# Kernel tuning notes

Measured on AMD Instinct MI355X. Metric: run time of the kernel, lower is better.

Reference implementation:

```python
import jax, jax.numpy as jnp
import numpy as np

D_MODEL = 768
D_STATE = 16
D_CONV = 4
EXPAND = 2
D_INNER = EXPAND * D_MODEL  # 1536
DT_RANK = 48  # ceil(768/16)
D_FF = 3072
EPS = 1e-5


def layer_norm(x, g, b):
    mu = jnp.mean(x, axis=-1, keepdims=True)
    var = jnp.mean((x - mu) ** 2, axis=-1, keepdims=True)
    return (x - mu) * jax.lax.rsqrt(var + EPS) * g + b


def selective_scan(u, delta, A, Bm, Cm, Dp, delta_bias):
    # u, delta: (B, d, L); A: (d, n); Bm, Cm: (B, n, L); Dp: (d,)
    delta = jax.nn.softplus(delta + delta_bias[None, :, None])
    dT = jnp.moveaxis(delta, 2, 0)  # (L, B, d)
    uT = jnp.moveaxis(u, 2, 0)      # (L, B, d)
    BT = jnp.moveaxis(Bm, 2, 0)     # (L, B, n)
    CT = jnp.moveaxis(Cm, 2, 0)     # (L, B, n)

    def step(h, inp):
        d_t, u_t, b_t, c_t = inp
        dA = jnp.exp(d_t[:, :, None] * A)                      # (B, d, n)
        h = dA * h + (d_t * u_t)[:, :, None] * b_t[:, None, :]  # (B, d, n)
        y = jnp.einsum('bdn,bn->bd', h, c_t)
        return h, y

    h0 = jnp.zeros((u.shape[0], A.shape[0], A.shape[1]), u.dtype)
    _, ys = jax.lax.scan(step, h0, (dT, uT, BT, CT))  # ys: (L, B, d)
    y = jnp.moveaxis(ys, 0, 2)  # (B, d, L)
    return y + u * Dp[None, :, None]


def mamba_mixer(x, in_proj_w, conv_w, conv_b, x_proj_w, dt_proj_w, dt_proj_b,
                A_log, D_param, out_proj_w):
    # x: (B, L, d_model)
    B, L, _ = x.shape
    x_and_res = x @ in_proj_w.T                      # (B, L, 2*d_inner)
    xs, res = jnp.split(x_and_res, [D_INNER], axis=-1)
    xi = jnp.transpose(xs, (0, 2, 1))                # (B, d_inner, L)
    # causal depthwise conv (torch pads d_conv-1 both sides then slices [:L])
    xi = jax.lax.conv_general_dilated(
        xi, conv_w, window_strides=(1,), padding=[(D_CONV - 1, 0)],
        feature_group_count=D_INNER,
        dimension_numbers=('NCH', 'OIH', 'NCH')) + conv_b[None, :, None]
    xs = jax.nn.silu(jnp.transpose(xi, (0, 2, 1)))   # (B, L, d_inner)
    # SSM
    proj = xs @ x_proj_w.T                           # (B, L, dt_rank + 2n)
    dt, Bm, Cm = jnp.split(proj, [DT_RANK, DT_RANK + D_STATE], axis=-1)
    delta = jnp.einsum('blr,dr->bdl', dt, dt_proj_w)  # (B, d_inner, L)
    A = -jnp.exp(A_log)                               # (d_inner, n)
    y = selective_scan(jnp.transpose(xs, (0, 2, 1)), delta, A,
                       jnp.transpose(Bm, (0, 2, 1)), jnp.transpose(Cm, (0, 2, 1)),
                       D_param, dt_proj_b)            # (B, d_inner, L)
    y = jnp.transpose(y, (0, 2, 1)) * jax.nn.silu(res)
    return y @ out_proj_w.T                           # (B, L, d_model)


def setup_inputs() -> dict:
    key = jax.random.key(0)
    ks = jax.random.split(key, 16)
    s = 0.02
    src = jax.random.normal(ks[0], (4, 8, 128, D_MODEL), jnp.float32)
    in_proj_w = jax.random.normal(ks[1], (2 * D_INNER, D_MODEL), jnp.float32) * s
    conv_w = jax.random.normal(ks[2], (D_INNER, 1, D_CONV), jnp.float32) * 0.2
    conv_b = jnp.zeros((D_INNER,), jnp.float32)
    x_proj_w = jax.random.normal(ks[3], (DT_RANK + 2 * D_STATE, D_INNER), jnp.float32) * s
    dt_std = DT_RANK ** -0.5
    dt_proj_w = jax.random.uniform(ks[4], (D_INNER, DT_RANK), jnp.float32, -dt_std, dt_std)
    dt = jnp.exp(jax.random.uniform(ks[5], (D_INNER,), jnp.float32) *
                 (np.log(0.1) - np.log(0.001)) + np.log(0.001))
    dt = jnp.clip(dt, 1e-4, None)
    dt_proj_b = dt + jnp.log(-jnp.expm1(-dt))
    A_log = jnp.log(jnp.broadcast_to(jnp.arange(1, D_STATE + 1, dtype=jnp.float32),
                                     (D_INNER, D_STATE)))
    D_param = jnp.ones((D_INNER,), jnp.float32)
    out_proj_w = jax.random.normal(ks[6], (D_MODEL, D_INNER), jnp.float32) * s
    return {
        'src': src,
        'norm1_g': jnp.ones((D_MODEL,), jnp.float32), 'norm1_b': jnp.zeros((D_MODEL,), jnp.float32),
        'in_proj_w': in_proj_w, 'conv_w': conv_w, 'conv_b': conv_b,
        'x_proj_w': x_proj_w, 'dt_proj_w': dt_proj_w, 'dt_proj_b': dt_proj_b,
        'A_log': A_log, 'D_param': D_param, 'out_proj_w': out_proj_w,
        'norm2_g': jnp.ones((D_MODEL,), jnp.float32), 'norm2_b': jnp.zeros((D_MODEL,), jnp.float32),
        'w1': jax.random.normal(ks[7], (D_FF, D_MODEL), jnp.float32) * s,
        'b1': jnp.zeros((D_FF,), jnp.float32),
        'w2': jax.random.normal(ks[8], (D_MODEL, D_FF), jnp.float32) * s,
        'b2': jnp.zeros((D_MODEL,), jnp.float32),
    }


def reference(src, norm1_g, norm1_b, in_proj_w, conv_w, conv_b, x_proj_w,
              dt_proj_w, dt_proj_b, A_log, D_param, out_proj_w,
              norm2_g, norm2_b, w1, b1, w2, b2):
    Bz, Ch, P, Dm = src.shape
    x = src
    # pre-norm mixer block (dropout=0 / eval)
    h = layer_norm(x, norm1_g, norm1_b).reshape(Bz, Ch * P, Dm)
    m = mamba_mixer(h, in_proj_w, conv_w, conv_b, x_proj_w, dt_proj_w,
                    dt_proj_b, A_log, D_param, out_proj_w).reshape(Bz, Ch, P, Dm)
    x = x + m
    # pre-norm FFN block (exact GELU like torch F.gelu default)
    h2 = layer_norm(x, norm2_g, norm2_b)
    ff = jax.nn.gelu(h2 @ w1.T + b1, approximate=False) @ w2.T + b2
    return x + ff
```

## Files before the change

### kernel.cpp

```cpp
#include <hip/hip_runtime.h>
#include <cstdint>
#include <cstddef>

typedef __attribute__((ext_vector_type(4))) float f32x4;
typedef __attribute__((ext_vector_type(8))) short s16x8;

#if __has_builtin(__builtin_amdgcn_exp2f)
#define EXP2F(x) __builtin_amdgcn_exp2f(x)
#else
#define EXP2F(x) __expf((x) * 0.6931471805599453f)
#endif
#if __has_builtin(__builtin_amdgcn_rcpf)
#define RCPF(x) __builtin_amdgcn_rcpf(x)
#else
#define RCPF(x) (1.0f / (x))
#endif

__device__ inline unsigned short f2b(float f) {
  union { float f; unsigned u; } c; c.f = f;
  return (unsigned short)((c.u + 0x7FFFu + ((c.u >> 16) & 1u)) >> 16);
}
__device__ inline float b2f(unsigned short u) {
  union { unsigned u; float f; } c; c.u = ((unsigned)u) << 16;
  return c.f;
}

__device__ inline void gload_lds16(const void* g, void* l) {
  __builtin_amdgcn_global_load_lds(
      (const __attribute__((address_space(1))) unsigned int*)g,
      (__attribute__((address_space(3))) unsigned int*)l, 16, 0, 0);
}

#define RAW_BARRIER() asm volatile("s_barrier" ::: "memory")

#define HOLE2 6291456
__device__ inline size_t hole(int j) {
  int r = j / 1536;
  int c = j - r * 1536;
  return (size_t)r * 3072 + c;
}

__global__ __launch_bounds__(256) void cvt_all(const float* __restrict__ inW,
                                               const float* __restrict__ outW,
                                               const float* __restrict__ w1,
                                               const float* __restrict__ w2,
                                               unsigned short* __restrict__ wbA,
                                               unsigned short* __restrict__ wbO,
                                               unsigned short* __restrict__ wb1,
                                               unsigned short* __restrict__ wb2) {
  int i = blockIdx.x * 256 + threadIdx.x;
  const float* src;
  unsigned short* dst;
  int o;
  if (i < 589824)       { src = inW;  dst = wbA; o = i; }
  else if (i < 884736)  { src = outW; dst = wbO; o = i - 589824; }
  else if (i < 1474560) { src = w1;   dst = wb1; o = i - 884736; }
  else                  { src = w2;   dst = wb2; o = i - 1474560; }
  float4 v = ((const float4*)src)[o];
  ushort4 u;
  u.x = f2b(v.x); u.y = f2b(v.y); u.z = f2b(v.z); u.w = f2b(v.w);
  ((ushort4*)dst)[o] = u;
}

__global__ __launch_bounds__(256) void build_proj(const float* __restrict__ xpw,
                                                  const float* __restrict__ dtw,
                                                  unsigned short* __restrict__ wpad,
                                                  unsigned short* __restrict__ wdt) {
  int i = blockIdx.x * 256 + threadIdx.x;
  if (i < 196608) {
    int row = i / 1536;
    wpad[i] = (row < 80) ? f2b(xpw[i]) : (unsigned short)0;
  } else {
    int j = i - 196608;
    int row = j >> 6, k = j & 63;
    wdt[j] = (k < 48) ? f2b(dtw[row * 48 + k]) : (unsigned short)0;
  }
}

__global__ __launch_bounds__(256) void reduce_projA(const float* __restrict__ Pa,
                                                    unsigned short* __restrict__ dtbf,
                                                    float* __restrict__ projBC) {
  int i = blockIdx.x * 256 + threadIdx.x;
  int row = i >> 7, col = i & 127;
  float s = Pa[i] + Pa[i + 524288] + Pa[i + 1048576] + Pa[i + 1572864];
  if (col < 48) {
    dtbf[row * 64 + col] = f2b(s);
  } else if (col < 64) {
    dtbf[row * 64 + col] = 0;
    projBC[row * 32 + col - 48] = s;
  } else if (col < 80) {
    projBC[row * 32 + col - 48] = s;
  }
}

__global__ __launch_bounds__(256) void ln_kernel(const float* __restrict__ x,
                                                 const float* __restrict__ gam,
                                                 const float* __restrict__ bet,
                                                 unsigned short* __restrict__ out) {
  int w = threadIdx.x >> 6, lane = threadIdx.x & 63;
  size_t row = (size_t)blockIdx.x * 4 + w;
  const float4* xr = (const float4*)(x + row * 768);
  float4 v0 = xr[lane], v1 = xr[lane + 64], v2 = xr[lane + 128];
  float s = v0.x + v0.y + v0.z + v0.w + v1.x + v1.y + v1.z + v1.w +
            v2.x + v2.y + v2.z + v2.w;
  #pragma unroll
  for (int o = 32; o; o >>= 1) s += __shfl_xor(s, o);
  float mu = s * (1.f / 768.f);
  float q = 0.f;
  {
    float d;
    d = v0.x - mu; q += d * d; d = v0.y - mu; q += d * d;
    d = v0.z - mu; q += d * d; d = v0.w - mu; q += d * d;
    d = v1.x - mu; q += d * d; d = v1.y - mu; q += d * d;
    d = v1.z - mu; q += d * d; d = v1.w - mu; q += d * d;
    d = v2.x - mu; q += d * d; d = v2.y - mu; q += d * d;
    d = v2.z - mu; q += d * d; d = v2.w - mu; q += d * d;
  }
  #pragma unroll
  for (int o = 32; o; o >>= 1) q += __shfl_xor(q, o);
  float rs = rsqrtf(q * (1.f / 768.f) + 1e-5f);
  const float4* gr = (const float4*)gam;
  const float4* br = (const float4*)bet;
  ushort4* orow = (ushort4*)(out + row * 768);
  float4 vv[3] = {v0, v1, v2};
  #pragma unroll
  for (int i = 0; i < 3; ++i) {
    int c4 = lane + i * 64;
    float4 g4 = gr[c4], b4 = br[c4];
    ushort4 o;
    o.x = f2b((vv[i].x - mu) * rs * g4.x + b4.x);
    o.y = f2b((vv[i].y - mu) * rs * g4.y + b4.y);
    o.z = f2b((vv[i].z - mu) * rs * g4.z + b4.z);
    o.w = f2b((vv[i].w - mu) * rs * g4.w + b4.w);
    orow[c4] = o;
  }
}

__global__ __launch_bounds__(256) void reduce_ln(
    const float* __restrict__ Pp, const float* __restrict__ src,
    const float* __restrict__ gam, const float* __restrict__ bet,
    float* __restrict__ xbuf, unsigned short* __restrict__ hbf) {
  int w = threadIdx.x >> 6, lane = threadIdx.x & 63;
  size_t row = (size_t)blockIdx.x * 4 + w;
  const float4* s4 = (const float4*)(src + row * 768);
  const float4* p0 = (const float4*)(Pp + row * 768);
  const float4* p1 = (const float4*)(Pp + 3145728 + row * 768);
  float4* xb4 = (float4*)(xbuf + row * 768);
  float4 xv[3];
  float s = 0.f;
  #pragma unroll
  for (int j = 0; j < 3; ++j) {
    int c4 = lane + j * 64;
    float4 a = s4[c4], b = p0[c4], c = p1[c4];
    float4 x;
    x.x = a.x + b.x + c.x; x.y = a.y + b.y + c.y;
    x.z = a.z + b.z + c.z; x.w = a.w + b.w + c.w;
    xv[j] = x;
    xb4[c4] = x;
    s += x.x + x.y + x.z + x.w;
  }
  #pragma unroll
  for (int o = 32; o; o >>= 1) s += __shfl_xor(s, o);
  float mu = s * (1.f / 768.f);
  float q = 0.f;
  #pragma unroll
  for (int j = 0; j < 3; ++j) {
    float d;
    d = xv[j].x - mu; q += d * d; d = xv[j].y - mu; q += d * d;
    d = xv[j].z - mu; q += d * d; d = xv[j].w - mu; q += d * d;
  }
  #pragma unroll
  for (int o = 32; o; o >>= 1) q += __shfl_xor(q, o);
  float rs = rsqrtf(q * (1.f / 768.f) + 1e-5f);
  const float4* gr = (const float4*)gam;
  const float4* br = (const float4*)bet;
  ushort4* orow = (ushort4*)(hbf + row * 768);
  #pragma unroll
  for (int j = 0; j < 3; ++j) {
    int c4 = lane + j * 64;
    float4 g4 = gr[c4], b4 = br[c4];
    ushort4 o;
    o.x = f2b((xv[j].x - mu) * rs * g4.x + b4.x);
    o.y = f2b((xv[j].y - mu) * rs * g4.y + b4.y);
    o.z = f2b((xv[j].z - mu) * rs * g4.z + b4.z);
    o.w = f2b((xv[j].w - mu) * rs * g4.w + b4.w);
    orow[c4] = o;
  }
}

__global__ __launch_bounds__(256) void reduce_out(
    const float* __restrict__ Pp, const float* __restrict__ xbuf,
    const float* __restrict__ bias, float* __restrict__ outp) {
  int i = blockIdx.x * 256 + threadIdx.x;
  int r = i / 192;
  int c4 = i - r * 192;
  float4 b4 = ((const float4*)bias)[c4];
  float4 x = ((const float4*)xbuf)[i];
  float4 p0 = ((const float4*)Pp)[i];
  float4 p1 = ((const float4*)(Pp + 3145728))[i];
  float4 o;
  o.x = x.x + b4.x + p0.x + p1.x;
  o.y = x.y + b4.y + p0.y + p1.y;
  o.z = x.z + b4.z + p0.z + p1.z;
  o.w = x.w + b4.w + p0.w + p1.w;
  ((float4*)outp)[i] = o;
}

__global__ __launch_bounds__(256) void conv_silu(const float* __restrict__ xres,
                                                 const float* __restrict__ cw,
                                                 const float* __restrict__ cb,
                                                 unsigned short* __restrict__ xs_act) {
  int idx = blockIdx.x * 256 + threadIdx.x;
  int t = idx / 384;
  int c4 = idx - t * 384;
  int pos = t & 1023;
  const float* base = xres + (size_t)t * 3072 + c4 * 4;
  float4 z = {0.f, 0.f, 0.f, 0.f};
  float4 x3 = *(const float4*)base;
  float4 x2 = (pos >= 1) ? *(const float4*)(base - 3072) : z;
  float4 x1 = (pos >= 2) ? *(const float4*)(base - 6144) : z;
  float4 x0 = (pos >= 3) ? *(const float4*)(base - 9216) : z;
  float a0[4] = {x0.x, x0.y, x0.z, x0.w};
  float a1[4] = {x1.x, x1.y, x1.z, x1.w};
  float a2[4] = {x2.x, x2.y, x2.z, x2.w};
  float a3[4] = {x3.x, x3.y, x3.z, x3.w};
  ushort4 o;
  unsigned short* op = &o.x;
  #pragma unroll
  for (int i = 0; i < 4; ++i) {
    int dd = c4 * 4 + i;
    float4 wv = *(const float4*)(cw + dd * 4);
    float v = wv.x * a0[i] + wv.y * a1[i] + wv.z * a2[i] + wv.w * a3[i] + cb[dd];
    float sv = v * RCPF(1.f + __expf(-v));
    op[i] = f2b(sv);
  }
  *(ushort4*)(xs_act + (size_t)t * 1536 + c4 * 4) = o;
}

__global__ __launch_bounds__(256) void scan_p1(
    const float* __restrict__ dsp, const unsigned short* __restrict__ u_bf,
    const float* __restrict__ projBC, const float* __restrict__ A_log,
    float* __restrict__ xdead) {
  int tid = threadIdx.x;
  int dl = tid >> 1;
  int nh = (tid & 1) * 8;
  int blk = blockIdx.x;
  int c = blk & 31;
  int bt = blk >> 5;
  int b = bt / 12;
  int dtile = bt - b * 12;
  int d = dtile * 128 + dl;
  float Al2[8];
  {
    float4 a0 = *(const float4*)(A_log + d * 16 + nh);
    float4 a1 = *(const float4*)(A_log + d * 16 + nh + 4);
    const float L2E = 1.4426950408889634f;
    Al2[0] = -__expf(a0.x) * L2E; Al2[1] = -__expf(a0.y) * L2E;
    Al2[2] = -__expf(a0.z) * L2E; Al2[3] = -__expf(a0.w) * L2E;
    Al2[4] = -__expf(a1.x) * L2E; Al2[5] = -__expf(a1.y) * L2E;
    Al2[6] = -__expf(a1.z) * L2E; Al2[7] = -__expf(a1.w) * L2E;
  }
  const float* base_d = dsp + (size_t)b * 1024 * 1536 + d;
  const float* base_bc = projBC + (size_t)b * 1024 * 32 + nh;
  const unsigned short* ub = u_bf + (size_t)b * 1024 * 1536 + d;
  float h[8];
  #pragma unroll
  for (int k = 0; k < 8; ++k) h[k] = 0.f;
  float S = 0.f;
  int t0 = c * 32;
  float dspA = base_d[(size_t)t0 * 1536];
  float utA = b2f(ub[(size_t)t0 * 1536]);
  float4 B0A = *(const float4*)(base_bc + (size_t)t0 * 32);
  float4 B1A = *(const float4*)(base_bc + (size_t)t0 * 32 + 4);
  float dspB, utB;
  float4 B0B, B1B;
#define P1_BODY(DSP, UT, B0, B1)                                   \
  {                                                                \
    S += DSP;                                                      \
    float du = DSP * UT;                                           \
    float Bv[8] = {B0.x, B0.y, B0.z, B0.w, B1.x, B1.y, B1.z, B1.w};\
    _Pragma("unroll")                                              \
    for (int k = 0; k < 8; ++k) {                                  \
      float dA = EXP2F(DSP * Al2[k]);                              \
      h[k] = __builtin_fmaf(dA, h[k], du * Bv[k]);                 \
    }                                                              \
  }
  for (int s = 0; s < 32; s += 2) {
    size_t t1 = t0 + s + 1;
    dspB = base_d[t1 * 1536];
    utB = b2f(ub[t1 * 1536]);
    B0B = *(const float4*)(base_bc + t1 * 32);
    B1B = *(const float4*)(base_bc + t1 * 32 + 4);
    P1_BODY(dspA, utA, B0A, B1A);
    int t2i = t0 + s + 2; if (t2i > 1023) t2i = 1023;
    size_t t2 = t2i;
    dspA = base_d[t2 * 1536];
    utA = b2f(ub[t2 * 1536]);
    B0A = *(const float4*)(base_bc + t2 * 32);
    B1A = *(const float4*)(base_bc + t2 * 32 + 4);
    P1_BODY(dspB, utB, B0B, B1B);
  }
#undef P1_BODY
  int j = c * 98304 + (b * 1536 + d) * 16 + nh;
  size_t hp = hole(j);
  xdead[hp]     = EXP2F(Al2[0] * S);
  xdead[hp + 1] = EXP2F(Al2[1] * S);
  xdead[hp + 2] = EXP2F(Al2[2] * S);
  xdead[hp + 3] = EXP2F(Al2[3] * S);
  xdead[hp + 4] = EXP2F(Al2[4] * S);
  xdead[hp + 5] = EXP2F(Al2[5] * S);
  xdead[hp + 6] = EXP2F(Al2[6] * S);
  xdead[hp + 7] = EXP2F(Al2[7] * S);
  float* he = xdead + hp + HOLE2;
  *(float4*)he = make_float4(h[0], h[1], h[2], h[3]);
  *(float4*)(he + 4) = make_float4(h[4], h[5], h[6], h[7]);
}

__global__ __launch_bounds__(256) void scan_p2(float* __restrict__ xdead) {
  int i = blockIdx.x * 256 + threadIdx.x;
  float H = 0.f;
  #pragma unroll
  for (int c = 0; c < 32; ++c) {
    int j = c * 98304 + i;
    size_t hp = hole(j);
    float P = xdead[hp];
    float he = xdead[hp + HOLE2];
    xdead[hp] = H;
    H = __builtin_fmaf(P, H, he);
  }
}

__global__ __launch_bounds__(256) void scan_p3(
    const float* __restrict__ dsp, const unsigned short* __restrict__ u_bf,
    const float* __restrict__ projBC, const float* __restrict__ xres,
    const float* __restrict__ A_log, const float* __restrict__ D_param,
    unsigned short* __restrict__ y_out) {
  int tid = threadIdx.x;
  int dl = tid >> 1;
  int nh = (tid & 1) * 8;
  int blk = blockIdx.x;
  int c = blk & 31;
  int bt = blk >> 5;
  int b = bt / 12;
  int dtile = bt - b * 12;
  int d = dtile * 128 + dl;
  float Dp = D_param[d];
  float Al2[8];
  {
    float4 a0 = *(const float4*)(A_log + d * 16 + nh);
    float4 a1 = *(const float4*)(A_log + d * 16 + nh + 4);
    const float L2E = 1.4426950408889634f;
    Al2[0] = -__expf(a0.x) * L2E; Al2[1] = -__expf(a0.y) * L2E;
    Al2[2] = -__expf(a0.z) * L2E; Al2[3] = -__expf(a0.w) * L2E;
    Al2[4] = -__expf(a1.x) * L2E; Al2[5] = -__expf(a1.y) * L2E;
    Al2[6] = -__expf(a1.z) * L2E; Al2[7] = -__expf(a1.w) * L2E;
  }
  const float* base_d = dsp + (size_t)b * 1024 * 1536 + d;
  const float* base_bc = projBC + (size_t)b * 1024 * 32 + nh;
  const unsigned short* ub = u_bf + (size_t)b * 1024 * 1536 + d;
  const float* rbase = xres + (size_t)b * 1024 * 3072 + 1536 + d;
  unsigned short* yrow = y_out + (size_t)b * 1024 * 1536 + d;
  int j = c * 98304 + (b * 1536 + d) * 16 + nh;
  float h[8];
  {
    size_t hp = hole(j);
    float4 h0 = *(const float4*)(xres + hp);
    float4 h1 = *(const float4*)(xres + hp + 4);
    h[0] = h0.x; h[1] = h0.y; h[2] = h0.z; h[3] = h0.w;
    h[4] = h1.x; h[5] = h1.y; h[6] = h1.z; h[7] = h1.w;
  }
  int t0 = c * 32;
  float dspA = base_d[(size_t)t0 * 1536];
  float utA = b2f(ub[(size_t)t0 * 1536]);
  float4 B0A = *(const float4*)(base_bc + (size_t)t0 * 32);
  float4 B1A = *(const float4*)(base_bc + (size_t)t0 * 32 + 4);
  float4 C0A = *(const float4*)(base_bc + (size_t)t0 * 32 + 16);
  float4 C1A = *(const float4*)(base_bc + (size_t)t0 * 32 + 20);
  float rA = rbase[(size_t)t0 * 3072];
  float dspB, utB, rB;
  float4 B0B, B1B, C0B, C1B;
#define P3_BODY(DSP, UT, B0, B1, C0, C1, RV, TT)                   \
  {                                                                \
    float du = DSP * UT;                                           \
    float Bv[8] = {B0.x, B0.y, B0.z, B0.w, B1.x, B1.y, B1.z, B1.w};\
    float Cv[8] = {C0.x, C0.y, C0.z, C0.w, C1.x, C1.y, C1.z, C1.w};\
    float p0 = 0.f, p1v = 0.f;                                     \
    _Pragma("unroll")                                              \
    for (int k = 0; k < 8; ++k) {                                  \
      float dA = EXP2F(DSP * Al2[k]);                              \
      h[k] = __builtin_fmaf(dA, h[k], du * Bv[k]);                 \
      if (k & 1) p1v = __builtin_fmaf(h[k], Cv[k], p1v);           \
      else       p0  = __builtin_fmaf(h[k], Cv[k], p0);            \
    }                                                              \
    float p = p0 + p1v;                                            \
    p += __int_as_float(__builtin_amdgcn_update_dpp(               \
        0, __float_as_int(p), 0xB1, 0xF, 0xF, true));              \
    if (nh == 0) {                                                 \
      float sr = RV * RCPF(1.f + __expf(-RV));                     \
      yrow[(size_t)(TT) * 1536] = f2b(__builtin_fmaf(UT, Dp, p) * sr); \
    }                                                              \
  }
  for (int s = 0; s < 32; s += 2) {
    size_t t1 = t0 + s + 1;
    dspB = base_d[t1 * 1536];
    utB = b2f(ub[t1 * 1536]);
    B0B = *(const float4*)(base_bc + t1 * 32);
    B1B = *(const float4*)(base_bc + t1 * 32 + 4);
    C0B = *(const float4*)(base_bc + t1 * 32 + 16);
    C1B = *(const float4*)(base_bc + t1 * 32 + 20);
    rB = rbase[t1 * 3072];
    P3_BODY(dspA, utA, B0A, B1A, C0A, C1A, rA, t0 + s);
    int t2i = t0 + s + 2; if (t2i > 1023) t2i = 1023;
    size_t t2 = t2i;
    dspA = base_d[t2 * 1536];
    utA = b2f(ub[t2 * 1536]);
    B0A = *(const float4*)(base_bc + t2 * 32);
    B1A = *(const float4*)(base_bc + t2 * 32 + 4);
    C0A = *(const float4*)(base_bc + t2 * 32 + 16);
    C1A = *(const float4*)(base_bc + t2 * 32 + 20);
    rA = rbase[t2 * 3072];
    P3_BODY(dspB, utB, B0B, B1B, C0B, C1B, rB, t1);
  }
#undef P3_BODY
}

template <int MODE, int BM>
__global__ __launch_bounds__(256, 2) void gemm_bt(
    const unsigned short* __restrict__ A, const unsigned short* __restrict__ B,
    int M, int N, int K, float* __restrict__ Cf, unsigned short* __restrict__ Cb,
    const float* __restrict__ res, const float* __restrict__ bias) {
  constexpr int NFR = (BM == 128) ? 4 : 2;
  constexpr int AIT = BM / 64;
  __shared__ __align__(16) unsigned short As[2][BM * 32];
  __shared__ __align__(16) unsigned short Bs[2][128 * 32];
  int tid = threadIdx.x;
  int lane = tid & 63;
  int w = tid >> 6;
  int wm = (BM == 128) ? (w >> 1) : 0;
  int wn = (BM == 128) ? (w & 1) : w;
  int row0 = blockIdx.x * BM;
  int col0 = blockIdx.y * 128;
  const int lr = lane & 15;
  const int kb = lane >> 4;
  int ksl = K / gridDim.z;
  int kbeg = blockIdx.z * ksl;

  f32x4 acc[4][NFR];
  #pragma unroll
  for (int i = 0; i < 4; ++i)
    #pragma unroll
    for (int j = 0; j < NFR; ++j) acc[i][j] = (f32x4)0.f;

  auto stage = [&](int buf, int k0) {
    #pragma unroll
    for (int j = 0; j < AIT; ++j) {
      int e = j * 256 + tid;
      int r = e >> 2, cc = e & 3;
      int sc = cc ^ ((r >> 1) & 3);
      gload_lds16(A + (size_t)(row0 + r) * K + k0 + sc * 8, &As[buf][e * 8]);
    }
    #pragma unroll
    for (int j = 0; j < 2; ++j) {
      int e = j * 256 + tid;
      int r = e >> 2, cc = e & 3;
      int sc = cc ^ ((r >> 1) & 3);
      gload_lds16(B + (size_t)(col0 + r) * K + k0 + sc * 8, &Bs[buf][e * 8]);
    }
  };

  int nt = ksl >> 5;
  stage(0, kbeg);
  if (nt > 1) stage(1, kbeg + 32);

  int cur = 0;
  for (int t = 0; t < nt; ++t) {
    if (t + 1 < nt) {
      if (BM == 128) asm volatile("s_waitcnt vmcnt(4)" ::: "memory");
      else           asm volatile("s_waitcnt vmcnt(3)" ::: "memory");
    } else {
      asm volatile("s_waitcnt vmcnt(0)" ::: "memory");
    }
    RAW_BARRIER();
    s16x8 af[4], bfm[NFR];
    #pragma unroll
    for (int m = 0; m < 4; ++m) {
      int rr = wm * 64 + m * 16 + lr;
      int chunk = rr * 4 + (kb ^ ((rr >> 1) & 3));
      af[m] = *(const s16x8*)&As[cur][chunk * 8];
    }
    #pragma unroll
    for (int nn = 0; nn < NFR; ++nn) {
      int rr = wn * (16 * NFR) + nn * 16 + lr;
      int chunk = rr * 4 + (kb ^ ((rr >> 1) & 3));
      bfm[nn] = *(const s16x8*)&Bs[cur][chunk * 8];
    }
    #pragma unroll
    for (int m = 0; m < 4; ++m)
      #pragma unroll
      for (int nn = 0; nn < NFR; ++nn)
        acc[m][nn] = __builtin_amdgcn_mfma_f32_16x16x32_bf16(af[m], bfm[nn], acc[m][nn], 0, 0, 0);
    RAW_BARRIER();
    if (t + 2 < nt) stage(cur, kbeg + ((t + 2) << 5));
    cur ^= 1;
  }

  size_t zoff = (size_t)blockIdx.z * M * N;
  #pragma unroll
  for (int m = 0; m < 4; ++m) {
    int rbase = row0 + wm * 64 + m * 16 + kb * 4;
    #pragma unroll
    for (int nn = 0; nn < NFR; ++nn) {
      int col = col0 + wn * (16 * NFR) + nn * 16 + lr;
      #pragma unroll
      for (int r = 0; r < 4; ++r) {
        int row = rbase + r;
        size_t idx = (size_t)row * N + col;
        float v = acc[m][nn][r];
        if (MODE == 0) {
          Cf[idx] = v;
        } else if (MODE == 2) {
          float tt = v + bias[col];
          float gl = 0.5f * tt * (1.f + erff(tt * 0.7071067811865475f));
          Cb[idx] = f2b(gl);
        } else if (MODE == 5) {
          Cf[zoff + idx] = v;
        } else {
          float xx = v + bias[col];
          Cf[idx] = (xx > 20.f) ? xx : __logf(1.f + __expf(xx));
        }
      }
    }
  }
}

extern "C" void kernel_launch(void* const* d_in, const int* in_sizes, int n_in,
                              void* d_out, int out_size, void* d_ws, size_t ws_size,
                              hipStream_t stream) {
  (void)in_sizes; (void)n_in; (void)out_size; (void)ws_size;
  const float* src   = (const float*)d_in[0];
  const float* n1g   = (const float*)d_in[1];
  const float* n1b   = (const float*)d_in[2];
  const float* inW   = (const float*)d_in[3];
  const float* convW = (const float*)d_in[4];
  const float* convB = (const float*)d_in[5];
  const float* xpW   = (const float*)d_in[6];
  const float* dtW   = (const float*)d_in[7];
  const float* dtB   = (const float*)d_in[8];
  const float* Alog  = (const float*)d_in[9];
  const float* Dpar  = (const float*)d_in[10];
  const float* outW  = (const float*)d_in[11];
  const float* n2g   = (const float*)d_in[12];
  const float* n2b   = (const float*)d_in[13];
  const float* w1    = (const float*)d_in[14];
  const float* b1    = (const float*)d_in[15];
  const float* w2    = (const float*)d_in[16];
  const float* b2    = (const float*)d_in[17];

  char* ws = (char*)d_ws;
  unsigned short* wbA   = (unsigned short*)(ws + 0);
  unsigned short* wbO   = (unsigned short*)(ws + 4718592);
  unsigned short* wb1   = (unsigned short*)(ws + 7077888);
  unsigned short* wb2   = (unsigned short*)(ws + 11796480);
  unsigned short* wpad  = (unsigned short*)(ws + 16515072);
  unsigned short* wdt   = (unsigned short*)(ws + 16908288);
  unsigned short* hbf   = (unsigned short*)(ws + 21626880);
  float*          xres  = (float*)(ws + 27918336);
  float*          Ppart = (float*)(ws + 27918336);
  unsigned short* xsact = (unsigned short*)(ws + 78249984);
  float*          xbuf  = (float*)(ws + 78249984);
  float*          dsp   = (float*)(ws + 90832896);
  unsigned short* ff1   = (unsigned short*)(ws + 90832896);
  float*          projBC= (float*)(ws + 115998720);
  unsigned short* dtbf  = (unsigned short*)(ws + 116523008);
  float*          Pa    = (float*)(ws + 118095872);
  unsigned short* ybuf  = (unsigned short*)(ws + 118095872);
  float* outp = (float*)d_out;

  cvt_all<<<8064, 256, 0, stream>>>(inW, outW, w1, w2, wbA, wbO, wb1, wb2);
  build_proj<<<1152, 256, 0, stream>>>(xpW, dtW, wpad, wdt);

  ln_kernel<<<1024, 256, 0, stream>>>(src, n1g, n1b, hbf);
  gemm_bt<0, 128><<<dim3(32, 24), 256, 0, stream>>>(hbf, wbA, 4096, 3072, 768, xres, nullptr, nullptr, nullptr);
  conv_silu<<<6144, 256, 0, stream>>>(xres, convW, convB, xsact);

  gemm_bt<5, 64><<<dim3(64, 1, 4), 256, 0, stream>>>(xsact, wpad, 4096, 128, 1536, Pa, nullptr, nullptr, nullptr);
  reduce_projA<<<2048, 256, 0, stream>>>(Pa, dtbf, projBC);
  gemm_bt<6, 128><<<dim3(32, 12), 256, 0, stream>>>(dtbf, wdt, 4096, 1536, 64, dsp, nullptr, nullptr, dtB);

  scan_p1<<<1536, 256, 0, stream>>>(dsp, xsact, projBC, Alog, xres);
  scan_p2<<<384, 256, 0, stream>>>(xres);
  scan_p3<<<1536, 256, 0, stream>>>(dsp, xsact, projBC, xres, Alog, Dpar, ybuf);

  gemm_bt<5, 64><<<dim3(64, 6, 2), 256, 0, stream>>>(ybuf, wbO, 4096, 768, 1536, Ppart, nullptr, nullptr, nullptr);
  reduce_ln<<<1024, 256, 0, stream>>>(Ppart, src, n2g, n2b, xbuf, hbf);

  gemm_bt<2, 128><<<dim3(32, 24), 256, 0, stream>>>(hbf, wb1, 4096, 3072, 768, nullptr, ff1, nullptr, b1);
  gemm_bt<5, 64><<<dim3(64, 6, 2), 256, 0, stream>>>(ff1, wb2, 4096, 768, 3072, Ppart, nullptr, nullptr, nullptr);
  reduce_out<<<3072, 256, 0, stream>>>(Ppart, xbuf, b2, outp);
}
```

Measured before the change: 262.7 us.

## Store in_proj and delta outputs as bf16, split scan buffers, triple-buffer GEMM

```diff
diff --git a/kernel.cpp b/kernel.cpp
--- a/kernel.cpp
+++ b/kernel.cpp
@@ -32,13 +32,6 @@
 }
 
 #define RAW_BARRIER() asm volatile("s_barrier" ::: "memory")
-
-#define HOLE2 6291456
-__device__ inline size_t hole(int j) {
-  int r = j / 1536;
-  int c = j - r * 1536;
-  return (size_t)r * 3072 + c;
-}
 
 __global__ __launch_bounds__(256) void cvt_all(const float* __restrict__ inW,
                                                const float* __restrict__ outW,
@@ -206,7 +199,7 @@
   ((float4*)outp)[i] = o;
 }
 
-__global__ __launch_bounds__(256) void conv_silu(const float* __restrict__ xres,
+__global__ __launch_bounds__(256) void conv_silu(const unsigned short* __restrict__ xs_pre,
                                                  const float* __restrict__ cw,
                                                  const float* __restrict__ cb,
                                                  unsigned short* __restrict__ xs_act) {
@@ -214,16 +207,16 @@
   int t = idx / 384;
   int c4 = idx - t * 384;
   int pos = t & 1023;
-  const float* base = xres + (size_t)t * 3072 + c4 * 4;
-  float4 z = {0.f, 0.f, 0.f, 0.f};
-  float4 x3 = *(const float4*)base;
-  float4 x2 = (pos >= 1) ? *(const float4*)(base - 3072) : z;
-  float4 x1 = (pos >= 2) ? *(const float4*)(base - 6144) : z;
-  float4 x0 = (pos >= 3) ? *(const float4*)(base - 9216) : z;
-  float a0[4] = {x0.x, x0.y, x0.z, x0.w};
-  float a1[4] = {x1.x, x1.y, x1.z, x1.w};
-  float a2[4] = {x2.x, x2.y, x2.z, x2.w};
-  float a3[4] = {x3.x, x3.y, x3.z, x3.w};
+  const unsigned short* base = xs_pre + (size_t)t * 1536 + c4 * 4;
+  ushort4 z = {0, 0, 0, 0};
+  ushort4 x3 = *(const ushort4*)base;
+  ushort4 x2 = (pos >= 1) ? *(const ushort4*)(base - 1536) : z;
+  ushort4 x1 = (pos >= 2) ? *(const ushort4*)(base - 3072) : z;
+  ushort4 x0 = (pos >= 3) ? *(const ushort4*)(base - 4608) : z;
+  float a0[4] = {b2f(x0.x), b2f(x0.y), b2f(x0.z), b2f(x0.w)};
+  float a1[4] = {b2f(x1.x), b2f(x1.y), b2f(x1.z), b2f(x1.w)};
+  float a2[4] = {b2f(x2.x), b2f(x2.y), b2f(x2.z), b2f(x2.w)};
+  float a3[4] = {b2f(x3.x), b2f(x3.y), b2f(x3.z), b2f(x3.w)};
   ushort4 o;
   unsigned short* op = &o.x;
   #pragma unroll
@@ -238,9 +231,9 @@
 }
 
 __global__ __launch_bounds__(256) void scan_p1(
-    const float* __restrict__ dsp, const unsigned short* __restrict__ u_bf,
+    const unsigned short* __restrict__ dsp, const unsigned short* __restrict__ u_bf,
     const float* __restrict__ projBC, const float* __restrict__ A_log,
-    float* __restrict__ xdead) {
+    float* __restrict__ Pbuf, float* __restrict__ Hbuf) {
   int tid = threadIdx.x;
   int dl = tid >> 1;
   int nh = (tid & 1) * 8;
@@ -260,7 +253,7 @@
     Al2[4] = -__expf(a1.x) * L2E; Al2[5] = -__expf(a1.y) * L2E;
     Al2[6] = -__expf(a1.z) * L2E; Al2[7] = -__expf(a1.w) * L2E;
   }
-  const float* base_d = dsp + (size_t)b * 1024 * 1536 + d;
+  const unsigned short* base_d = dsp + (size_t)b * 1024 * 1536 + d;
   const float* base_bc = projBC + (size_t)b * 1024 * 32 + nh;
   const unsigned short* ub = u_bf + (size_t)b * 1024 * 1536 + d;
   float h[8];
@@ -268,7 +261,7 @@
   for (int k = 0; k < 8; ++k) h[k] = 0.f;
   float S = 0.f;
   int t0 = c * 32;
-  float dspA = base_d[(size_t)t0 * 1536];
+  float dspA = b2f(base_d[(size_t)t0 * 1536]);
   float utA = b2f(ub[(size_t)t0 * 1536]);
   float4 B0A = *(const float4*)(base_bc + (size_t)t0 * 32);
   float4 B1A = *(const float4*)(base_bc + (size_t)t0 * 32 + 4);
@@ -287,14 +280,14 @@
   }
   for (int s = 0; s < 32; s += 2) {
     size_t t1 = t0 + s + 1;
-    dspB = base_d[t1 * 1536];
+    dspB = b2f(base_d[t1 * 1536]);
     utB = b2f(ub[t1 * 1536]);
     B0B = *(const float4*)(base_bc + t1 * 32);
     B1B = *(const float4*)(base_bc + t1 * 32 + 4);
     P1_BODY(dspA, utA, B0A, B1A);
     int t2i = t0 + s + 2; if (t2i > 1023) t2i = 1023;
     size_t t2 = t2i;
-    dspA = base_d[t2 * 1536];
+    dspA = b2f(base_d[t2 * 1536]);
     utA = b2f(ub[t2 * 1536]);
     B0A = *(const float4*)(base_bc + t2 * 32);
     B1A = *(const float4*)(base_bc + t2 * 32 + 4);
@@ -302,39 +295,35 @@
   }
 #undef P1_BODY
   int j = c * 98304 + (b * 1536 + d) * 16 + nh;
-  size_t hp = hole(j);
-  xdead[hp]     = EXP2F(Al2[0] * S);
-  xdead[hp + 1] = EXP2F(Al2[1] * S);
-  xdead[hp + 2] = EXP2F(Al2[2] * S);
-  xdead[hp + 3] = EXP2F(Al2[3] * S);
-  xdead[hp + 4] = EXP2F(Al2[4] * S);
-  xdead[hp + 5] = EXP2F(Al2[5] * S);
-  xdead[hp + 6] = EXP2F(Al2[6] * S);
-  xdead[hp + 7] = EXP2F(Al2[7] * S);
-  float* he = xdead + hp + HOLE2;
-  *(float4*)he = make_float4(h[0], h[1], h[2], h[3]);
-  *(float4*)(he + 4) = make_float4(h[4], h[5], h[6], h[7]);
-}
-
-__global__ __launch_bounds__(256) void scan_p2(float* __restrict__ xdead) {
+  float4 P0 = make_float4(EXP2F(Al2[0] * S), EXP2F(Al2[1] * S),
+                          EXP2F(Al2[2] * S), EXP2F(Al2[3] * S));
+  float4 P1 = make_float4(EXP2F(Al2[4] * S), EXP2F(Al2[5] * S),
+                          EXP2F(Al2[6] * S), EXP2F(Al2[7] * S));
+  *(float4*)(Pbuf + j) = P0;
+  *(float4*)(Pbuf + j + 4) = P1;
+  *(float4*)(Hbuf + j) = make_float4(h[0], h[1], h[2], h[3]);
+  *(float4*)(Hbuf + j + 4) = make_float4(h[4], h[5], h[6], h[7]);
+}
+
+__global__ __launch_bounds__(256) void scan_p2(float* __restrict__ Pbuf,
+                                               const float* __restrict__ Hbuf) {
   int i = blockIdx.x * 256 + threadIdx.x;
   float H = 0.f;
   #pragma unroll
   for (int c = 0; c < 32; ++c) {
     int j = c * 98304 + i;
-    size_t hp = hole(j);
-    float P = xdead[hp];
-    float he = xdead[hp + HOLE2];
-    xdead[hp] = H;
+    float P = Pbuf[j];
+    float he = Hbuf[j];
+    Pbuf[j] = H;
     H = __builtin_fmaf(P, H, he);
   }
 }
 
 __global__ __launch_bounds__(256) void scan_p3(
-    const float* __restrict__ dsp, const unsigned short* __restrict__ u_bf,
-    const float* __restrict__ projBC, const float* __restrict__ xres,
+    const unsigned short* __restrict__ dsp, const unsigned short* __restrict__ u_bf,
+    const float* __restrict__ projBC, const unsigned short* __restrict__ res_pre,
     const float* __restrict__ A_log, const float* __restrict__ D_param,
-    unsigned short* __restrict__ y_out) {
+    const float* __restrict__ Pbuf, unsigned short* __restrict__ y_out) {
   int tid = threadIdx.x;
   int dl = tid >> 1;
   int nh = (tid & 1) * 8;
@@ -355,28 +344,27 @@
     Al2[4] = -__expf(a1.x) * L2E; Al2[5] = -__expf(a1.y) * L2E;
     Al2[6] = -__expf(a1.z) * L2E; Al2[7] = -__expf(a1.w) * L2E;
   }
-  const float* base_d = dsp + (size_t)b * 1024 * 1536 + d;
+  const unsigned short* base_d = dsp + (size_t)b * 1024 * 1536 + d;
   const float* base_bc = projBC + (size_t)b * 1024 * 32 + nh;
   const unsigned short* ub = u_bf + (size_t)b * 1024 * 1536 + d;
-  const float* rbase = xres + (size_t)b * 1024 * 3072 + 1536 + d;
+  const unsigned short* rbase = res_pre + (size_t)b * 1024 * 1536 + d;
   unsigned short* yrow = y_out + (size_t)b * 1024 * 1536 + d;
   int j = c * 98304 + (b * 1536 + d) * 16 + nh;
   float h[8];
   {
-    size_t hp = hole(j);
-    float4 h0 = *(const float4*)(xres + hp);
-    float4 h1 = *(const float4*)(xres + hp + 4);
+    float4 h0 = *(const float4*)(Pbuf + j);
+    float4 h1 = *(const float4*)(Pbuf + j + 4);
     h[0] = h0.x; h[1] = h0.y; h[2] = h0.z; h[3] = h0.w;
     h[4] = h1.x; h[5] = h1.y; h[6] = h1.z; h[7] = h1.w;
   }
   int t0 = c * 32;
-  float dspA = base_d[(size_t)t0 * 1536];
+  float dspA = b2f(base_d[(size_t)t0 * 1536]);
   float utA = b2f(ub[(size_t)t0 * 1536]);
   float4 B0A = *(const float4*)(base_bc + (size_t)t0 * 32);
   float4 B1A = *(const float4*)(base_bc + (size_t)t0 * 32 + 4);
   float4 C0A = *(const float4*)(base_bc + (size_t)t0 * 32 + 16);
   float4 C1A = *(const float4*)(base_bc + (size_t)t0 * 32 + 20);
-  float rA = rbase[(size_t)t0 * 3072];
+  float rA = b2f(rbase[(size_t)t0 * 1536]);
   float dspB, utB, rB;
   float4 B0B, B1B, C0B, C1B;
 #define P3_BODY(DSP, UT, B0, B1, C0, C1, RV, TT)                   \
@@ -402,23 +390,23 @@
   }
   for (int s = 0; s < 32; s += 2) {
     size_t t1 = t0 + s + 1;
-    dspB = base_d[t1 * 1536];
+    dspB = b2f(base_d[t1 * 1536]);
     utB = b2f(ub[t1 * 1536]);
     B0B = *(const float4*)(base_bc + t1 * 32);
     B1B = *(const float4*)(base_bc + t1 * 32 + 4);
     C0B = *(const float4*)(base_bc + t1 * 32 + 16);
     C1B = *(const float4*)(base_bc + t1 * 32 + 20);
-    rB = rbase[t1 * 3072];
+    rB = b2f(rbase[t1 * 1536]);
     P3_BODY(dspA, utA, B0A, B1A, C0A, C1A, rA, t0 + s);
     int t2i = t0 + s + 2; if (t2i > 1023) t2i = 1023;
     size_t t2 = t2i;
-    dspA = base_d[t2 * 1536];
+    dspA = b2f(base_d[t2 * 1536]);
     utA = b2f(ub[t2 * 1536]);
     B0A = *(const float4*)(base_bc + t2 * 32);
     B1A = *(const float4*)(base_bc + t2 * 32 + 4);
     C0A = *(const float4*)(base_bc + t2 * 32 + 16);
     C1A = *(const float4*)(base_bc + t2 * 32 + 20);
-    rA = rbase[t2 * 3072];
+    rA = b2f(rbase[t2 * 1536]);
     P3_BODY(dspB, utB, B0B, B1B, C0B, C1B, rB, t1);
   }
 #undef P3_BODY
@@ -431,8 +419,9 @@
     const float* __restrict__ res, const float* __restrict__ bias) {
   constexpr int NFR = (BM == 128) ? 4 : 2;
   constexpr int AIT = BM / 64;
-  __shared__ __align__(16) unsigned short As[2][BM * 32];
-  __shared__ __align__(16) unsigned short Bs[2][128 * 32];
+  constexpr int NB  = (BM == 128) ? 3 : 2;
+  __shared__ __align__(16) unsigned short As[NB][BM * 32];
+  __shared__ __align__(16) unsigned short Bs[NB][128 * 32];
   int tid = threadIdx.x;
   int lane = tid & 63;
   int w = tid >> 6;
@@ -471,14 +460,18 @@
   int nt = ksl >> 5;
   stage(0, kbeg);
   if (nt > 1) stage(1, kbeg + 32);
+  if (NB > 2 && nt > 2) stage(2, kbeg + 64);
 
   int cur = 0;
   for (int t = 0; t < nt; ++t) {
-    if (t + 1 < nt) {
-      if (BM == 128) asm volatile("s_waitcnt vmcnt(4)" ::: "memory");
-      else           asm volatile("s_waitcnt vmcnt(3)" ::: "memory");
+    int rem = nt - 1 - t;
+    if (NB == 3) {
+      if (rem >= 2)      asm volatile("s_waitcnt vmcnt(8)" ::: "memory");
+      else if (rem == 1) asm volatile("s_waitcnt vmcnt(4)" ::: "memory");
+      else               asm volatile("s_waitcnt vmcnt(0)" ::: "memory");
     } else {
-      asm volatile("s_waitcnt vmcnt(0)" ::: "memory");
+      if (rem >= 1) asm volatile("s_waitcnt vmcnt(3)" ::: "memory");
+      else          asm volatile("s_waitcnt vmcnt(0)" ::: "memory");
     }
     RAW_BARRIER();
     s16x8 af[4], bfm[NFR];
@@ -500,8 +493,8 @@
       for (int nn = 0; nn < NFR; ++nn)
         acc[m][nn] = __builtin_amdgcn_mfma_f32_16x16x32_bf16(af[m], bfm[nn], acc[m][nn], 0, 0, 0);
     RAW_BARRIER();
-    if (t + 2 < nt) stage(cur, kbeg + ((t + 2) << 5));
-    cur ^= 1;
+    if (t + NB < nt) stage(cur, kbeg + ((t + NB) << 5));
+    cur = (cur + 1 == NB) ? 0 : cur + 1;
   }
 
   size_t zoff = (size_t)blockIdx.z * M * N;
@@ -516,17 +509,22 @@
         int row = rbase + r;
         size_t idx = (size_t)row * N + col;
         float v = acc[m][nn][r];
-        if (MODE == 0) {
-          Cf[idx] = v;
-        } else if (MODE == 2) {
+        if (MODE == 2) {
           float tt = v + bias[col];
           float gl = 0.5f * tt * (1.f + erff(tt * 0.7071067811865475f));
           Cb[idx] = f2b(gl);
         } else if (MODE == 5) {
           Cf[zoff + idx] = v;
+        } else if (MODE == 6) {
+          float xx = v + bias[col];
+          float sp = (xx > 20.f) ? xx : __logf(1.f + __expf(xx));
+          Cb[idx] = f2b(sp);
         } else {
-          float xx = v + bias[col];
-          Cf[idx] = (xx > 20.f) ? xx : __logf(1.f + __expf(xx));
+          if (col < 1536) {
+            Cb[(size_t)row * 1536 + col] = f2b(v);
+          } else {
+            ((unsigned short*)Cf)[(size_t)row * 1536 + col - 1536] = f2b(v);
+          }
         }
       }
     }
@@ -564,11 +562,14 @@
   unsigned short* wpad  = (unsigned short*)(ws + 16515072);
   unsigned short* wdt   = (unsigned short*)(ws + 16908288);
   unsigned short* hbf   = (unsigned short*)(ws + 21626880);
-  float*          xres  = (float*)(ws + 27918336);
-  float*          Ppart = (float*)(ws + 27918336);
+  unsigned short* xs_pre= (unsigned short*)(ws + 27918336);
+  unsigned short* res_pre=(unsigned short*)(ws + 40501248);
+  float*          Pbuf  = (float*)(ws + 53084160);
+  float*          Hbuf  = (float*)(ws + 65667072);
+  float*          Ppart = (float*)(ws + 53084160);
   unsigned short* xsact = (unsigned short*)(ws + 78249984);
   float*          xbuf  = (float*)(ws + 78249984);
-  float*          dsp   = (float*)(ws + 90832896);
+  unsigned short* dsp   = (unsigned short*)(ws + 90832896);
   unsigned short* ff1   = (unsigned short*)(ws + 90832896);
   float*          projBC= (float*)(ws + 115998720);
   unsigned short* dtbf  = (unsigned short*)(ws + 116523008);
@@ -580,16 +581,16 @@
   build_proj<<<1152, 256, 0, stream>>>(xpW, dtW, wpad, wdt);
 
   ln_kernel<<<1024, 256, 0, stream>>>(src, n1g, n1b, hbf);
-  gemm_bt<0, 128><<<dim3(32, 24), 256, 0, stream>>>(hbf, wbA, 4096, 3072, 768, xres, nullptr, nullptr, nullptr);
-  conv_silu<<<6144, 256, 0, stream>>>(xres, convW, convB, xsact);
+  gemm_bt<7, 128><<<dim3(32, 24), 256, 0, stream>>>(hbf, wbA, 4096, 3072, 768, (float*)res_pre, xs_pre, nullptr, nullptr);
+  conv_silu<<<6144, 256, 0, stream>>>(xs_pre, convW, convB, xsact);
 
   gemm_bt<5, 64><<<dim3(64, 1, 4), 256, 0, stream>>>(xsact, wpad, 4096, 128, 1536, Pa, nullptr, nullptr, nullptr);
   reduce_projA<<<2048, 256, 0, stream>>>(Pa, dtbf, projBC);
-  gemm_bt<6, 128><<<dim3(32, 12), 256, 0, stream>>>(dtbf, wdt, 4096, 1536, 64, dsp, nullptr, nullptr, dtB);
-
-  scan_p1<<<1536, 256, 0, stream>>>(dsp, xsact, projBC, Alog, xres);
-  scan_p2<<<384, 256, 0, stream>>>(xres);
-  scan_p3<<<1536, 256, 0, stream>>>(dsp, xsact, projBC, xres, Alog, Dpar, ybuf);
+  gemm_bt<6, 128><<<dim3(32, 12), 256, 0, stream>>>(dtbf, wdt, 4096, 1536, 64, nullptr, dsp, nullptr, dtB);
+
+  scan_p1<<<1536, 256, 0, stream>>>(dsp, xsact, projBC, Alog, Pbuf, Hbuf);
+  scan_p2<<<384, 256, 0, stream>>>(Pbuf, Hbuf);
+  scan_p3<<<1536, 256, 0, stream>>>(dsp, xsact, projBC, res_pre, Alog, Dpar, Pbuf, ybuf);
 
   gemm_bt<5, 64><<<dim3(64, 6, 2), 256, 0, stream>>>(ybuf, wbO, 4096, 768, 1536, Ppart, nullptr, nullptr, nullptr);
   reduce_ln<<<1024, 256, 0, stream>>>(Ppart, src, n2g, n2b, xbuf, hbf);
```

Result: faster. 256.3 us (-2.4%).
